# Performance work log

Measured on AMD Instinct MI355X. Metric: run time of the kernel, lower is better.

## Reference

```python
import jax, jax.numpy as jnp
import numpy as np

B, D, H, K = 16384, 128, 1024, 8
OPD = 3 * K + 1  # params per dim
TB = 3.0         # tail_bound: left=bottom=-TB, right=top=TB
EPS = 1e-12
MIN_W = MIN_H = MIN_D = 1e-3


def _masks():
    rng = np.random.RandomState(0)
    in_deg = np.arange(1, D + 1)
    h1 = rng.randint(1, D, size=(H,))
    h2 = rng.randint(1, D, size=(H,))
    out_deg = np.arange(1, D + 1)
    m1 = (in_deg[None, :] <= h1[:, None]).astype(np.float32)          # [H, D]
    m2 = (h1[None, :] <= h2[:, None]).astype(np.float32)              # [H, H]
    m3 = np.repeat((out_deg[:, None] > h2[None, :]).astype(np.float32), OPD, axis=0)  # [D*OPD, H]
    return jnp.asarray(m1), jnp.asarray(m2), jnp.asarray(m3)


def _kaiming(key, fan_out, fan_in, a=0.1):
    bound = np.sqrt(6.0 / ((1.0 + a * a) * fan_in))
    return jax.random.uniform(key, (fan_out, fan_in), jnp.float32, -bound, bound)


def setup_inputs() -> dict:
    key = jax.random.key(0)
    kx, k1, k2, k3 = jax.random.split(key, 4)
    m1, m2, m3 = _masks()
    return {
        'x': jax.random.normal(kx, (B, D), jnp.float32),
        'W1': _kaiming(k1, H, D), 'b1': jnp.zeros((H,), jnp.float32),
        'W2': _kaiming(k2, H, H), 'b2': jnp.zeros((H,), jnp.float32),
        'W3': _kaiming(k3, D * OPD, H), 'b3': jnp.zeros((D * OPD,), jnp.float32),
        'm1': m1, 'm2': m2, 'm3': m3,
    }


def _norm_cum(u, mn):
    k = u.shape[-1]
    w = jax.nn.softmax(u, axis=-1)
    w = mn + (1.0 - mn * k) * w
    c = jnp.cumsum(w, axis=-1)
    c = jnp.pad(c, [(0, 0)] * (c.ndim - 1) + [(1, 0)])
    c = c / jnp.clip(c[..., -1:], 1e-12)
    return c[..., 1:] - c[..., :-1], c


def _take(p, idx):
    return jnp.take_along_axis(p, idx[..., None], axis=-1)[..., 0]


def _forward(x, W1, b1, W2, b2, W3, b3, m1, m2, m3):
    h = jax.nn.silu(x @ (W1 * m1).T + b1)
    h = jax.nn.silu(h @ (W2 * m2).T + b2)
    raw = (h @ (W3 * m3).T + b3).reshape(-1, D, OPD)  # [B, D, 3K+1]
    uw, uh, ud = raw[..., :K], raw[..., K:2 * K], raw[..., 2 * K:]
    w, cw = _norm_cum(uw, MIN_W)
    hh, ch = _norm_cum(uh, MIN_H)
    d = MIN_D + jax.nn.softplus(ud)  # [B, D, K+1]

    left, right, bottom, top = -TB, TB, -TB, TB
    inside = (x >= left) & (x <= right)  # [B, D]
    xs = jnp.clip((x - left) / (right - left), 0.0, 1.0)
    bid = jnp.clip(jnp.sum((xs[..., None] >= cw), axis=-1) - 1, 0, K - 1)
    xk, wk = _take(cw, bid), _take(w, bid)
    yk, hk = _take(ch, bid), _take(hh, bid)
    dk, dk1 = _take(d, bid), _take(d, bid + 1)
    t = jnp.clip((xs - xk) / (wk + EPS), 0.0, 1.0)
    a = (hk + EPS) / (wk + EPS)
    num = a * t * t + dk * t * (1 - t)
    den = a + (dk + dk1 - 2 * a) * t * (1 - t)
    s = num / (den + EPS)
    y = (yk + hk * s) * (top - bottom) + bottom
    dnum = a * a * (dk1 * t * t + 2 * a * t * (1 - t) + dk * (1 - t) * (1 - t))
    dydx = (top - bottom) / (right - left) * dnum / (den * den + EPS)
    out = jnp.where(inside, y, x)
    lad = jnp.where(inside, jnp.log(jnp.clip(dydx, 1e-12)), 0.0)
    return out, jnp.sum(lad, axis=-1)


def reference(x, W1, b1, W2, b2, W3, b3, m1, m2, m3):
    return _forward(x, W1, b1, W2, b2, W3, b3, m1, m2, m3)
```

## Files before the change

### kernel.cpp

```cpp
#include <hip/hip_runtime.h>
#include <hip/hip_bf16.h>

#define BATCH 16384
#define DIM   128
#define HID   1024
#define NK    8
#define OPD   25
#define N3    (DIM*OPD)
#define NP    3328

typedef __attribute__((ext_vector_type(8))) short  short8;
typedef __attribute__((ext_vector_type(4))) float  floatx4;
typedef unsigned int u32;

__device__ __forceinline__ float fexp(float x) { return __expf(x); }
__device__ __forceinline__ float flog(float x) { return __logf(x); }
__device__ __forceinline__ float fdiv(float a, float b) { return __fdividef(a, b); }

__device__ __forceinline__ void async_copy16(const unsigned short* g,
                                             unsigned short* l) {
    __builtin_amdgcn_global_load_lds(
        (const __attribute__((address_space(1))) u32*)g,
        (__attribute__((address_space(3))) u32*)l,
        16, 0, 0);
}

__global__ __launch_bounds__(256) void pre_kernel(
    const float* __restrict__ m1, const float* __restrict__ m3,
    const float* __restrict__ x,
    int* __restrict__ h1i, int* __restrict__ h2i,
    __hip_bfloat16* __restrict__ xb, float* __restrict__ lad)
{
    const int b = blockIdx.x, t = threadIdx.x;
    if (b < 512) {
        const int row = 2 * b + (t >> 7);
        const int col = t & 127;
        float v = m1[row * DIM + col];
        #pragma unroll
        for (int off = 32; off > 0; off >>= 1) v += __shfl_down(v, off, 64);
        __shared__ float ws[4];
        if ((t & 63) == 0) ws[t >> 6] = v;
        __syncthreads();
        if (t == 0)   h1i[2 * b]     = (int)(ws[0] + ws[1] + 0.5f);
        if (t == 128) h1i[2 * b + 1] = (int)(ws[2] + ws[3] + 0.5f);
    } else if (b < 516) {
        const int j = (b - 512) * 256 + t;
        float s = 0.f;
        for (int d = 0; d < DIM; d++) s += m3[(size_t)d * OPD * HID + j];
        h2i[j] = DIM - (int)(s + 0.5f);
    } else {
        const int i = (b - 516) * 256 + t;
        xb[i] = __float2bfloat16(x[i]);
        if (i < BATCH) lad[i] = 0.f;
    }
}

__global__ __launch_bounds__(1024) void sort_kernel(
    const int* __restrict__ h1i, const int* __restrict__ h2i,
    int* __restrict__ perm1, int* __restrict__ perm2,
    int* __restrict__ h1sv, int* __restrict__ h2sv,
    int* __restrict__ klim1, int* __restrict__ klim2, int* __restrict__ klim3)
{
    __shared__ int hist[128];
    __shared__ int h1s[1024], h2s[1024];
    const int t = threadIdx.x;
    const int h1v = h1i[t], h2v = h2i[t];

    if (t < 128) hist[t] = 0;
    __syncthreads();
    atomicAdd(&hist[h1v], 1);
    __syncthreads();
    if (t == 0) { int a = 0; for (int b = 0; b < 128; b++) { int c = hist[b]; hist[b] = a; a += c; } }
    __syncthreads();
    int r = atomicAdd(&hist[h1v], 1);
    perm1[r] = t; h1s[r] = h1v; h1sv[r] = h1v;
    __syncthreads();
    if (t < 128) hist[t] = 0;
    __syncthreads();
    atomicAdd(&hist[h2v], 1);
    __syncthreads();
    if (t == 0) { int a = 0; for (int b = 0; b < 128; b++) { int c = hist[b]; hist[b] = a; a += c; } }
    __syncthreads();
    r = atomicAdd(&hist[h2v], 1);
    perm2[r] = t; h2s[r] = h2v; h2sv[r] = h2v;
    __syncthreads();

    if (t < 8) {
        klim1[t] = ((h1s[t * 128 + 127] + 63) >> 6) << 6;
        int mh = h2s[t * 128 + 127];
        int c = 0;
        for (int j = 0; j < 1024; j++) c += (h1s[j] <= mh) ? 1 : 0;
        klim2[t] = ((c + 63) >> 6) << 6;
    }
    if (t < 26) {
        int dmax = t * 5 + 4; if (dmax > 127) dmax = 127;
        int c = 0;
        for (int j = 0; j < 1024; j++) c += (h2s[j] <= dmax) ? 1 : 0;
        klim3[t] = ((c + 63) >> 6) << 6;
    }
}

__global__ __launch_bounds__(256) void megaprep_kernel(
    const float* __restrict__ W1, const float* __restrict__ b1,
    const float* __restrict__ W2, const float* __restrict__ b2,
    const float* __restrict__ W3,
    const int* __restrict__ perm1, const int* __restrict__ perm2,
    const int* __restrict__ h1sv, const int* __restrict__ h2sv,
    __hip_bfloat16* __restrict__ w1p, float* __restrict__ b1p,
    __hip_bfloat16* __restrict__ w2p, float* __restrict__ b2p,
    __hip_bfloat16* __restrict__ w3p)
{
    __shared__ float row[HID];
    const int b = blockIdx.x, t = threadIdx.x;
    if (b < HID) {
        const int si = perm2[b];
        const int h2v = h2sv[b];
        #pragma unroll
        for (int q = 0; q < 4; q++) row[q * 256 + t] = W2[(size_t)si * HID + q * 256 + t];
        __syncthreads();
        #pragma unroll
        for (int q = 0; q < 4; q++) {
            const int jp = q * 256 + t;
            float v = (h1sv[jp] <= h2v) ? row[perm1[jp]] : 0.f;
            w2p[(size_t)b * HID + jp] = __float2bfloat16(v);
        }
        if (t == 0) b2p[b] = b2[si];
    } else if (b < HID + NP) {
        const int c = b - HID;
        const int s = c & 127, t3 = c >> 7;
        if (s >= 125) {
            #pragma unroll
            for (int q = 0; q < 4; q++)
                w3p[(size_t)c * HID + q * 256 + t] = __float2bfloat16(0.f);
            return;
        }
        const int srcrow = t3 * 125 + s;
        const int d = srcrow / 25;
        #pragma unroll
        for (int q = 0; q < 4; q++) row[q * 256 + t] = W3[(size_t)srcrow * HID + q * 256 + t];
        __syncthreads();
        #pragma unroll
        for (int q = 0; q < 4; q++) {
            const int kk = q * 256 + t;
            float v = (h2sv[kk] <= d) ? row[perm2[kk]] : 0.f;
            w3p[(size_t)c * HID + kk] = __float2bfloat16(v);
        }
    } else {
        const int i = (b - HID - NP) * 256 + t;
        const int hp = i >> 7, col = i & 127;
        const int src = perm1[hp];
        float v = (col < h1sv[hp]) ? W1[src * DIM + col] : 0.f;
        w1p[i] = __float2bfloat16(v);
        if (col == 0) b1p[hp] = b1[src];
    }
}

__device__ __forceinline__ void spline_eval(const float* __restrict__ p,
                                            float xv, float& yout, float& lout) {
    float cw[NK + 1], ch[NK + 1];
    {
        float mx = p[0];
        #pragma unroll
        for (int j = 1; j < NK; j++) mx = fmaxf(mx, p[j]);
        float e[NK], s = 0.f;
        #pragma unroll
        for (int j = 0; j < NK; j++) { e[j] = fexp(p[j] - mx); s += e[j]; }
        const float inv = fdiv(1.f, s);
        cw[0] = 0.f;
        #pragma unroll
        for (int j = 0; j < NK; j++) cw[j + 1] = cw[j] + (0.001f + 0.992f * e[j] * inv);
    }
    {
        float mx = p[8];
        #pragma unroll
        for (int j = 1; j < NK; j++) mx = fmaxf(mx, p[8 + j]);
        float e[NK], s = 0.f;
        #pragma unroll
        for (int j = 0; j < NK; j++) { e[j] = fexp(p[8 + j] - mx); s += e[j]; }
        const float inv = fdiv(1.f, s);
        ch[0] = 0.f;
        #pragma unroll
        for (int j = 0; j < NK; j++) ch[j + 1] = ch[j] + (0.001f + 0.992f * e[j] * inv);
    }
    const float icw = fdiv(1.f, fmaxf(cw[NK], 1e-12f));
    const float ich = fdiv(1.f, fmaxf(ch[NK], 1e-12f));

    const bool inside = (xv >= -3.f) && (xv <= 3.f);
    float xs = (xv + 3.f) * (1.f / 6.f);
    xs = fminf(fmaxf(xs, 0.f), 1.f);
    const float xsc = xs * cw[NK];

    float xk = 0.f, wk = cw[1], yk = 0.f, hk = ch[1];
    float uda = p[16], udb = p[17];
    #pragma unroll
    for (int j = 1; j < NK; j++) {
        const bool c = (xsc >= cw[j]);
        xk  = c ? cw[j] : xk;
        wk  = c ? (cw[j + 1] - cw[j]) : wk;
        yk  = c ? ch[j] : yk;
        hk  = c ? (ch[j + 1] - ch[j]) : hk;
        uda = c ? p[16 + j] : uda;
        udb = c ? p[17 + j] : udb;
    }
    xk *= icw; wk *= icw;
    yk *= ich; hk *= ich;

    const float dk  = 0.001f + ((uda > 20.f) ? uda : flog(1.f + fexp(uda)));
    const float dk1 = 0.001f + ((udb > 20.f) ? udb : flog(1.f + fexp(udb)));

    float t = fdiv(xs - xk, wk + 1e-12f);
    t = fminf(fmaxf(t, 0.f), 1.f);
    const float a   = fdiv(hk + 1e-12f, wk + 1e-12f);
    const float omt = 1.f - t;
    const float tt1 = t * omt;
    const float num = a * t * t + dk * tt1;
    const float den = a + (dk + dk1 - 2.f * a) * tt1;
    const float s   = fdiv(num, den + 1e-12f);
    const float y   = (yk + hk * s) * 6.f - 3.f;
    const float dnum = a * a * (dk1 * t * t + 2.f * a * tt1 + dk * omt * omt);
    const float dydx = fdiv(dnum, den * den + 1e-12f);

    yout = inside ? y : xv;
    lout = inside ? flog(fmaxf(dydx, 1e-12f)) : 0.f;
}

__global__ __launch_bounds__(256, 4) void gemm_bt_kernel(
    const unsigned short* __restrict__ A,
    const unsigned short* __restrict__ Bw,
    const float* __restrict__ bias,
    const int* __restrict__ klim,
    __hip_bfloat16* __restrict__ Cout,
    int M, int N, int Kd)
{
    constexpr int BM = 128, BN = 128, BK = 64;
    __shared__ unsigned short As[BM * BK];
    __shared__ unsigned short Bs[BN * BK];

    const int bid = blockIdx.y * gridDim.x + blockIdx.x;
    const int GY  = (gridDim.y >= 16) ? 16 : gridDim.y;
    const int per_group = gridDim.x * GY;
    const int g  = bid / per_group;
    const int rr = bid % per_group;
    const int bn = (gridDim.x - 1 - rr / GY) * BN;
    const int bm = (g * GY + (rr % GY)) * BM;
    const int Klim = klim[bn >> 7];

    const int t    = threadIdx.x;
    const int lane = t & 63;
    const int w    = t >> 6;
    const int wr   = (w >> 1) * 64;
    const int wc   = (w & 1) * 64;
    const int lr   = lane & 15;
    const int quad = lane >> 4;
    const int lxor = lr & 7;

    floatx4 acc[4][4] = {};

    const int lrow = lane >> 3;
    const int lcol = ((lane & 7) ^ lrow) * 8;

    for (int k0 = 0; k0 < Klim; k0 += BK) {
        __syncthreads();
        #pragma unroll
        for (int p = 0; p < 4; p++) {
            const int q = w * 4 + p;
            const int r = q * 8 + lrow;
            async_copy16(&A[(size_t)(bm + r) * Kd + k0 + lcol],
                         &As[q * 512 + lane * 8]);
            async_copy16(&Bw[(size_t)(bn + r) * Kd + k0 + lcol],
                         &Bs[q * 512 + lane * 8]);
        }
        __syncthreads();
        #pragma unroll
        for (int ks = 0; ks < BK; ks += 32) {
            const int cbase = (ks >> 3) + quad;
            const int coff  = (cbase ^ lxor) * 8;
            short8 af[4], bfr[4];
            #pragma unroll
            for (int i = 0; i < 4; i++)
                af[i] = *(const short8*)&As[(wr + i * 16 + lr) * BK + coff];
            #pragma unroll
            for (int j = 0; j < 4; j++)
                bfr[j] = *(const short8*)&Bs[(wc + j * 16 + lr) * BK + coff];
            #pragma unroll
            for (int i = 0; i < 4; i++)
                #pragma unroll
                for (int j = 0; j < 4; j++)
                    acc[i][j] = __builtin_amdgcn_mfma_f32_16x16x32_bf16(
                        af[i], bfr[j], acc[i][j], 0, 0, 0);
        }
    }

    #pragma unroll
    for (int j = 0; j < 4; j++) {
        const int col = bn + wc + j * 16 + lr;
        const float bv = bias[col];
        #pragma unroll
        for (int i = 0; i < 4; i++) {
            const int rowb = bm + wr + i * 16 + quad * 4;
            #pragma unroll
            for (int r = 0; r < 4; r++) {
                float v = acc[i][j][r] + bv;
                v = v * fdiv(1.f, 1.f + fexp(-v));
                Cout[(size_t)(rowb + r) * N + col] = __float2bfloat16(v);
            }
        }
    }
}

__global__ __launch_bounds__(256, 4) void gemm3_spline_kernel(
    const unsigned short* __restrict__ A,
    const unsigned short* __restrict__ Bw,
    const float* __restrict__ b3,
    const int* __restrict__ klim,
    const float* __restrict__ x,
    float* __restrict__ out,
    float* __restrict__ lad,
    int M)
{
    constexpr int BM = 128, BN = 128, BK = 64, Kd = HID;
    constexpr int LSE = 133;
    __shared__ __align__(16) char smem[64 * LSE * 4 + 128 * 4];
    unsigned short* As = (unsigned short*)smem;
    unsigned short* Bs = (unsigned short*)(smem + BM * BK * 2);
    float* eb     = (float*)smem;
    float* ladacc = (float*)(smem + 64 * LSE * 4);

    const int bid = blockIdx.y * gridDim.x + blockIdx.x;
    const int GY  = 16;
    const int per_group = gridDim.x * GY;
    const int g  = bid / per_group;
    const int rr = bid % per_group;
    const int tile = 25 - rr / GY;
    const int bn = tile * BN;
    const int bm = (g * GY + (rr % GY)) * BM;
    const int Klim = klim[tile];

    const int t    = threadIdx.x;
    const int lane = t & 63;
    const int w    = t >> 6;
    const int wr   = (w >> 1) * 64;
    const int wc   = (w & 1) * 64;
    const int lr   = lane & 15;
    const int quad = lane >> 4;
    const int lxor = lr & 7;

    if (t < 128) ladacc[t] = 0.f;

    floatx4 acc[4][4] = {};

    const int lrow = lane >> 3;
    const int lcol = ((lane & 7) ^ lrow) * 8;

    for (int k0 = 0; k0 < Klim; k0 += BK) {
        __syncthreads();
        #pragma unroll
        for (int p = 0; p < 4; p++) {
            const int q = w * 4 + p;
            const int r = q * 8 + lrow;
            async_copy16(&A[(size_t)(bm + r) * Kd + k0 + lcol],
                         &As[q * 512 + lane * 8]);
            async_copy16(&Bw[(size_t)(bn + r) * Kd + k0 + lcol],
                         &Bs[q * 512 + lane * 8]);
        }
        __syncthreads();
        #pragma unroll
        for (int ks = 0; ks < BK; ks += 32) {
            const int cbase = (ks >> 3) + quad;
            const int coff  = (cbase ^ lxor) * 8;
            short8 af[4], bfr[4];
            #pragma unroll
            for (int i = 0; i < 4; i++)
                af[i] = *(const short8*)&As[(wr + i * 16 + lr) * BK + coff];
            #pragma unroll
            for (int j = 0; j < 4; j++)
                bfr[j] = *(const short8*)&Bs[(wc + j * 16 + lr) * BK + coff];
            #pragma unroll
            for (int i = 0; i < 4; i++)
                #pragma unroll
                for (int j = 0; j < 4; j++)
                    acc[i][j] = __builtin_amdgcn_mfma_f32_16x16x32_bf16(
                        af[i], bfr[j], acc[i][j], 0, 0, 0);
        }
    }

    #pragma unroll 1
    for (int h = 0; h < 2; h++) {
        __syncthreads();
        if ((w >> 1) == h) {
            #pragma unroll
            for (int j = 0; j < 4; j++) {
                const int s = wc + j * 16 + lr;
                const float bv = (s < 125) ? b3[tile * 125 + s] : 0.f;
                #pragma unroll
                for (int i = 0; i < 4; i++) {
                    const int lrw = i * 16 + quad * 4;
                    #pragma unroll
                    for (int r2 = 0; r2 < 4; r2++)
                        eb[(lrw + r2) * LSE + s] = acc[i][j][r2] + bv;
                }
            }
        }
        __syncthreads();
        #pragma unroll 1
        for (int q = t; q < 320; q += 256) {
            const int r  = q / 5;
            const int ds = q % 5;
            const int dim = tile * 5 + ds;
            if (dim < DIM) {
                const float* p = eb + r * LSE + ds * 25;
                const int grow = bm + h * 64 + r;
                const float xv = x[(size_t)grow * DIM + dim];
                float y, l;
                spline_eval(p, xv, y, l);
                out[(size_t)grow * DIM + dim] = y;
                atomicAdd(&ladacc[h * 64 + r], l);
            }
        }
    }
    __syncthreads();
    if (t < 128) atomicAdd(&lad[bm + t], ladacc[t]);
}

extern "C" void kernel_launch(void* const* d_in, const int* in_sizes, int n_in,
                              void* d_out, int out_size, void* d_ws, size_t ws_size,
                              hipStream_t stream) {
    const float* x  = (const float*)d_in[0];
    const float* W1 = (const float*)d_in[1];
    const float* b1 = (const float*)d_in[2];
    const float* W2 = (const float*)d_in[3];
    const float* b2 = (const float*)d_in[4];
    const float* W3 = (const float*)d_in[5];
    const float* b3 = (const float*)d_in[6];
    const float* m1 = (const float*)d_in[7];
    const float* m3 = (const float*)d_in[9];

    char* ws = (char*)d_ws;
    const size_t OFF_W1B = 0;
    const size_t OFF_W2B = OFF_W1B + (size_t)HID * DIM * 2;
    const size_t OFF_W3P = OFF_W2B + (size_t)HID * HID * 2;
    const size_t OFF_XB  = OFF_W3P + (size_t)NP * HID * 2;
    const size_t OFF_H1B = OFF_XB  + (size_t)BATCH * DIM * 2;
    const size_t OFF_H2B = OFF_H1B + (size_t)BATCH * HID * 2;
    const size_t OFF_SML = OFF_H2B + (size_t)BATCH * HID * 2;

    __hip_bfloat16* w1p = (__hip_bfloat16*)(ws + OFF_W1B);
    __hip_bfloat16* w2p = (__hip_bfloat16*)(ws + OFF_W2B);
    __hip_bfloat16* w3p = (__hip_bfloat16*)(ws + OFF_W3P);
    __hip_bfloat16* xb  = (__hip_bfloat16*)(ws + OFF_XB);
    __hip_bfloat16* h1b = (__hip_bfloat16*)(ws + OFF_H1B);
    __hip_bfloat16* h2b = (__hip_bfloat16*)(ws + OFF_H2B);

    float* b1p   = (float*)(ws + OFF_SML);
    float* b2p   = b1p + HID;
    int*   h1i   = (int*)(b2p + HID);
    int*   h2i   = h1i + HID;
    int*   perm1 = h2i + HID;
    int*   perm2 = perm1 + HID;
    int*   h1sv  = perm2 + HID;
    int*   h2sv  = h1sv + HID;
    int*   klim1 = h2sv + HID;
    int*   klim2 = klim1 + 8;
    int*   klim3 = klim2 + 8;

    float* out_p = (float*)d_out;
    float* lad_p = out_p + (size_t)BATCH * DIM;

    pre_kernel<<<516 + (BATCH * DIM) / 256, 256, 0, stream>>>(
        m1, m3, x, h1i, h2i, xb, lad_p);
    sort_kernel<<<1, 1024, 0, stream>>>(h1i, h2i, perm1, perm2, h1sv, h2sv,
                                        klim1, klim2, klim3);
    megaprep_kernel<<<HID + NP + (HID * DIM) / 256, 256, 0, stream>>>(
        W1, b1, W2, b2, W3, perm1, perm2, h1sv, h2sv,
        w1p, b1p, w2p, b2p, w3p);

    gemm_bt_kernel<<<dim3(HID / 128, BATCH / 128), 256, 0, stream>>>(
        (const unsigned short*)xb, (const unsigned short*)w1p, b1p, klim1, h1b,
        BATCH, HID, DIM);
    gemm_bt_kernel<<<dim3(HID / 128, BATCH / 128), 256, 0, stream>>>(
        (const unsigned short*)h1b, (const unsigned short*)w2p, b2p, klim2, h2b,
        BATCH, HID, HID);
    gemm3_spline_kernel<<<dim3(NP / 128, BATCH / 128), 256, 0, stream>>>(
        (const unsigned short*)h2b, (const unsigned short*)w3p, b3, klim3, x,
        out_p, lad_p, BATCH);
}
```

Measured before the change: 281.3 us.

## Fold mask reductions into sort kernel and pad spline params for vector loads

Removes the separate pre_kernel launch. The m1/m3 mask-degree reductions now run inside the single-block sort kernel, and the x-to-bf16 conversion and lad zeroing move into the megaprep kernel as extra blocks. The spline epilogue buffer is re-laid out with a 28-float stride per dimension so spline_eval can read its parameters with float4 LDS loads. The cost is that the mask reductions now run serially on a single block, which could lengthen the sort kernel.

```diff
diff --git a/kernel.cpp b/kernel.cpp
--- a/kernel.cpp
+++ b/kernel.cpp
@@ -25,46 +25,32 @@
         16, 0, 0);
 }
 
-__global__ __launch_bounds__(256) void pre_kernel(
+__global__ __launch_bounds__(1024) void sort_kernel(
     const float* __restrict__ m1, const float* __restrict__ m3,
-    const float* __restrict__ x,
-    int* __restrict__ h1i, int* __restrict__ h2i,
-    __hip_bfloat16* __restrict__ xb, float* __restrict__ lad)
-{
-    const int b = blockIdx.x, t = threadIdx.x;
-    if (b < 512) {
-        const int row = 2 * b + (t >> 7);
-        const int col = t & 127;
-        float v = m1[row * DIM + col];
-        #pragma unroll
-        for (int off = 32; off > 0; off >>= 1) v += __shfl_down(v, off, 64);
-        __shared__ float ws[4];
-        if ((t & 63) == 0) ws[t >> 6] = v;
-        __syncthreads();
-        if (t == 0)   h1i[2 * b]     = (int)(ws[0] + ws[1] + 0.5f);
-        if (t == 128) h1i[2 * b + 1] = (int)(ws[2] + ws[3] + 0.5f);
-    } else if (b < 516) {
-        const int j = (b - 512) * 256 + t;
-        float s = 0.f;
-        for (int d = 0; d < DIM; d++) s += m3[(size_t)d * OPD * HID + j];
-        h2i[j] = DIM - (int)(s + 0.5f);
-    } else {
-        const int i = (b - 516) * 256 + t;
-        xb[i] = __float2bfloat16(x[i]);
-        if (i < BATCH) lad[i] = 0.f;
-    }
-}
-
-__global__ __launch_bounds__(1024) void sort_kernel(
-    const int* __restrict__ h1i, const int* __restrict__ h2i,
     int* __restrict__ perm1, int* __restrict__ perm2,
     int* __restrict__ h1sv, int* __restrict__ h2sv,
     int* __restrict__ klim1, int* __restrict__ klim2, int* __restrict__ klim3)
 {
     __shared__ int hist[128];
     __shared__ int h1s[1024], h2s[1024];
+    __shared__ int h1a[1024];
     const int t = threadIdx.x;
-    const int h1v = h1i[t], h2v = h2i[t];
+
+    {
+        const int wv = t >> 6, l = t & 63;
+        for (int i = 0; i < 64; i++) {
+            const int r = wv * 64 + i;
+            float v = m1[r * DIM + l] + m1[r * DIM + 64 + l];
+            #pragma unroll
+            for (int off = 32; off > 0; off >>= 1) v += __shfl_down(v, off, 64);
+            if (l == 0) h1a[r] = (int)(v + 0.5f);
+        }
+    }
+    float s2 = 0.f;
+    for (int d = 0; d < DIM; d++) s2 += m3[(size_t)d * OPD * HID + t];
+    const int h2v = DIM - (int)(s2 + 0.5f);
+    __syncthreads();
+    const int h1v = h1a[t];
 
     if (t < 128) hist[t] = 0;
     __syncthreads();
@@ -103,12 +89,13 @@
 __global__ __launch_bounds__(256) void megaprep_kernel(
     const float* __restrict__ W1, const float* __restrict__ b1,
     const float* __restrict__ W2, const float* __restrict__ b2,
-    const float* __restrict__ W3,
+    const float* __restrict__ W3, const float* __restrict__ x,
     const int* __restrict__ perm1, const int* __restrict__ perm2,
     const int* __restrict__ h1sv, const int* __restrict__ h2sv,
     __hip_bfloat16* __restrict__ w1p, float* __restrict__ b1p,
     __hip_bfloat16* __restrict__ w2p, float* __restrict__ b2p,
-    __hip_bfloat16* __restrict__ w3p)
+    __hip_bfloat16* __restrict__ w3p,
+    __hip_bfloat16* __restrict__ xb, float* __restrict__ lad)
 {
     __shared__ float row[HID];
     const int b = blockIdx.x, t = threadIdx.x;
@@ -145,38 +132,61 @@
             float v = (h2sv[kk] <= d) ? row[perm2[kk]] : 0.f;
             w3p[(size_t)c * HID + kk] = __float2bfloat16(v);
         }
-    } else {
+    } else if (b < HID + NP + 512) {
         const int i = (b - HID - NP) * 256 + t;
         const int hp = i >> 7, col = i & 127;
         const int src = perm1[hp];
         float v = (col < h1sv[hp]) ? W1[src * DIM + col] : 0.f;
         w1p[i] = __float2bfloat16(v);
         if (col == 0) b1p[hp] = b1[src];
+    } else {
+        const int i = (b - HID - NP - 512) * 256 + t;
+        xb[i] = __float2bfloat16(x[i]);
+        if (i < BATCH) lad[i] = 0.f;
     }
 }
 
 __device__ __forceinline__ void spline_eval(const float* __restrict__ p,
                                             float xv, float& yout, float& lout) {
+    const float4* pv = (const float4*)p;
+    float uw[NK], uh[NK], ud[NK + 1];
+    {
+        float4 a = pv[0], b = pv[1];
+        uw[0] = a.x; uw[1] = a.y; uw[2] = a.z; uw[3] = a.w;
+        uw[4] = b.x; uw[5] = b.y; uw[6] = b.z; uw[7] = b.w;
+    }
+    {
+        float4 a = pv[2], b = pv[3];
+        uh[0] = a.x; uh[1] = a.y; uh[2] = a.z; uh[3] = a.w;
+        uh[4] = b.x; uh[5] = b.y; uh[6] = b.z; uh[7] = b.w;
+    }
+    {
+        float4 a = pv[4], b = pv[5];
+        ud[0] = a.x; ud[1] = a.y; ud[2] = a.z; ud[3] = a.w;
+        ud[4] = b.x; ud[5] = b.y; ud[6] = b.z; ud[7] = b.w;
+        ud[8] = p[24];
+    }
+
     float cw[NK + 1], ch[NK + 1];
     {
-        float mx = p[0];
-        #pragma unroll
-        for (int j = 1; j < NK; j++) mx = fmaxf(mx, p[j]);
+        float mx = uw[0];
+        #pragma unroll
+        for (int j = 1; j < NK; j++) mx = fmaxf(mx, uw[j]);
         float e[NK], s = 0.f;
         #pragma unroll
-        for (int j = 0; j < NK; j++) { e[j] = fexp(p[j] - mx); s += e[j]; }
+        for (int j = 0; j < NK; j++) { e[j] = fexp(uw[j] - mx); s += e[j]; }
         const float inv = fdiv(1.f, s);
         cw[0] = 0.f;
         #pragma unroll
         for (int j = 0; j < NK; j++) cw[j + 1] = cw[j] + (0.001f + 0.992f * e[j] * inv);
     }
     {
-        float mx = p[8];
-        #pragma unroll
-        for (int j = 1; j < NK; j++) mx = fmaxf(mx, p[8 + j]);
+        float mx = uh[0];
+        #pragma unroll
+        for (int j = 1; j < NK; j++) mx = fmaxf(mx, uh[j]);
         float e[NK], s = 0.f;
         #pragma unroll
-        for (int j = 0; j < NK; j++) { e[j] = fexp(p[8 + j] - mx); s += e[j]; }
+        for (int j = 0; j < NK; j++) { e[j] = fexp(uh[j] - mx); s += e[j]; }
         const float inv = fdiv(1.f, s);
         ch[0] = 0.f;
         #pragma unroll
@@ -191,7 +201,7 @@
     const float xsc = xs * cw[NK];
 
     float xk = 0.f, wk = cw[1], yk = 0.f, hk = ch[1];
-    float uda = p[16], udb = p[17];
+    float uda = ud[0], udb = ud[1];
     #pragma unroll
     for (int j = 1; j < NK; j++) {
         const bool c = (xsc >= cw[j]);
@@ -199,8 +209,8 @@
         wk  = c ? (cw[j + 1] - cw[j]) : wk;
         yk  = c ? ch[j] : yk;
         hk  = c ? (ch[j + 1] - ch[j]) : hk;
-        uda = c ? p[16 + j] : uda;
-        udb = c ? p[17 + j] : udb;
+        uda = c ? ud[j] : uda;
+        udb = c ? ud[j + 1] : udb;
     }
     xk *= icw; wk *= icw;
     yk *= ich; hk *= ich;
@@ -319,12 +329,12 @@
     int M)
 {
     constexpr int BM = 128, BN = 128, BK = 64, Kd = HID;
-    constexpr int LSE = 133;
-    __shared__ __align__(16) char smem[64 * LSE * 4 + 128 * 4];
+    constexpr int RS = 140;
+    __shared__ __align__(16) char smem[64 * RS * 4 + 128 * 4];
     unsigned short* As = (unsigned short*)smem;
     unsigned short* Bs = (unsigned short*)(smem + BM * BK * 2);
     float* eb     = (float*)smem;
-    float* ladacc = (float*)(smem + 64 * LSE * 4);
+    float* ladacc = (float*)(smem + 64 * RS * 4);
 
     const int bid = blockIdx.y * gridDim.x + blockIdx.x;
     const int GY  = 16;
@@ -391,13 +401,16 @@
             #pragma unroll
             for (int j = 0; j < 4; j++) {
                 const int s = wc + j * 16 + lr;
-                const float bv = (s < 125) ? b3[tile * 125 + s] : 0.f;
-                #pragma unroll
-                for (int i = 0; i < 4; i++) {
-                    const int lrw = i * 16 + quad * 4;
+                if (s < 125) {
+                    const float bv = b3[tile * 125 + s];
+                    const int ds = s / 25, o = s - ds * 25;
                     #pragma unroll
-                    for (int r2 = 0; r2 < 4; r2++)
-                        eb[(lrw + r2) * LSE + s] = acc[i][j][r2] + bv;
+                    for (int i = 0; i < 4; i++) {
+                        const int lrw = i * 16 + quad * 4;
+                        #pragma unroll
+                        for (int r2 = 0; r2 < 4; r2++)
+                            eb[(lrw + r2) * RS + ds * 28 + o] = acc[i][j][r2] + bv;
+                    }
                 }
             }
         }
@@ -408,7 +421,7 @@
             const int ds = q % 5;
             const int dim = tile * 5 + ds;
             if (dim < DIM) {
-                const float* p = eb + r * LSE + ds * 25;
+                const float* p = eb + r * RS + ds * 28;
                 const int grow = bm + h * 64 + r;
                 const float xv = x[(size_t)grow * DIM + dim];
                 float y, l;
@@ -453,9 +466,7 @@
 
     float* b1p   = (float*)(ws + OFF_SML);
     float* b2p   = b1p + HID;
-    int*   h1i   = (int*)(b2p + HID);
-    int*   h2i   = h1i + HID;
-    int*   perm1 = h2i + HID;
+    int*   perm1 = (int*)(b2p + HID);
     int*   perm2 = perm1 + HID;
     int*   h1sv  = perm2 + HID;
     int*   h2sv  = h1sv + HID;
@@ -466,13 +477,11 @@
     float* out_p = (float*)d_out;
     float* lad_p = out_p + (size_t)BATCH * DIM;
 
-    pre_kernel<<<516 + (BATCH * DIM) / 256, 256, 0, stream>>>(
-        m1, m3, x, h1i, h2i, xb, lad_p);
-    sort_kernel<<<1, 1024, 0, stream>>>(h1i, h2i, perm1, perm2, h1sv, h2sv,
+    sort_kernel<<<1, 1024, 0, stream>>>(m1, m3, perm1, perm2, h1sv, h2sv,
                                         klim1, klim2, klim3);
-    megaprep_kernel<<<HID + NP + (HID * DIM) / 256, 256, 0, stream>>>(
-        W1, b1, W2, b2, W3, perm1, perm2, h1sv, h2sv,
-        w1p, b1p, w2p, b2p, w3p);
+    megaprep_kernel<<<HID + NP + 512 + (BATCH * DIM) / 256, 256, 0, stream>>>(
+        W1, b1, W2, b2, W3, x, perm1, perm2, h1sv, h2sv,
+        w1p, b1p, w2p, b2p, w3p, xb, lad_p);
 
     gemm_bt_kernel<<<dim3(HID / 128, BATCH / 128), 256, 0, stream>>>(
         (const unsigned short*)xb, (const unsigned short*)w1p, b1p, klim1, h1b,
```

New measurement: 307.5 us. +9.3%, slower.
